# Performance work log

Measured on AMD Instinct MI355X. Metric: run time of the kernel, lower is better.

## Reference

```python
import jax, jax.numpy as jnp
import numpy as np

N_FRAME = 100000
N_TFN = 25000
E = 2000000
NUM_RBF = 16
D_MIN, D_MAX = 0.0, 20.0
EPS = 1e-8


def _rbf(d):
    # GVP-style radial basis: [E] -> [E, NUM_RBF]
    mu = jnp.linspace(D_MIN, D_MAX, NUM_RBF, dtype=d.dtype)
    sigma = (D_MAX - D_MIN) / NUM_RBF
    return jnp.exp(-(((d[..., None] - mu) / sigma) ** 2))


def _sh(vec, dist):
    # component-normalized real spherical harmonics l=0,1,2 on unit vectors
    # (normalize=True, normalization='component': ||Y_l||^2 = 2l+1)
    r = vec / dist[..., None]
    x, y, z = r[..., 0], r[..., 1], r[..., 2]
    s3 = 1.7320508075688772   # sqrt(3)
    s5 = 2.23606797749979     # sqrt(5)
    s15 = 3.872983346207417   # sqrt(15)
    l0 = jnp.ones_like(x)
    sh = jnp.stack([
        l0,
        s3 * x, s3 * y, s3 * z,
        s15 * x * y,
        s15 * y * z,
        0.5 * s5 * (3.0 * z * z - 1.0),
        s15 * x * z,
        0.5 * s15 * (x * x - y * y),
    ], axis=-1)  # [E, 9]
    return sh


def _edge_feats(vec):
    # eps-shifted norm, exactly as torch.linalg.vector_norm(vec + eps)
    d = jnp.linalg.norm(vec + EPS, axis=-1)  # [E]
    return jnp.concatenate([_rbf(d), _sh(vec, d)], axis=-1)  # [E, NUM_RBF+9]


def setup_inputs() -> dict:
    key = jax.random.key(0)
    k1, k2, k3, k4 = jax.random.split(key, 4)
    trans = jax.random.normal(k1, (N_FRAME, 3), dtype=jnp.float32) * 10.0
    f2t = jax.random.randint(k2, (2, E), 0, N_TFN)
    t2t = jax.random.randint(k3, (2, E), 0, N_TFN)
    t2f = jax.random.randint(k4, (2, E), 0, N_TFN)
    return {"trans": trans, "frame2tfn_edge_index": f2t,
            "tfn2tfn_edge_index": t2t, "tfn2frame_edge_index": t2f,
            "n_tfn": N_TFN}


def reference(trans, frame2tfn_edge_index, tfn2tfn_edge_index, tfn2frame_edge_index, n_tfn):
    f_src, t_dst = frame2tfn_edge_index[0], frame2tfn_edge_index[1]
    # scatter-mean of frame translations onto coarse (tfn) nodes
    sums = jax.ops.segment_sum(trans[f_src], t_dst, num_segments=n_tfn)  # [n_tfn, 3]
    cnt = jax.ops.segment_sum(jnp.ones((f_src.shape[0],), trans.dtype), t_dst,
                              num_segments=n_tfn)
    tfn_x = sums / jnp.maximum(cnt, 1.0)[:, None]
    # per-edge-type gather -> distance vecs -> RBF + SH
    f2t_vec = trans[f_src] - tfn_x[t_dst]
    t2t_vec = tfn_x[tfn2tfn_edge_index[0]] - tfn_x[tfn2tfn_edge_index[1]]
    t2f_vec = tfn_x[tfn2frame_edge_index[0]] - trans[tfn2frame_edge_index[1]]
    out = jnp.stack([_edge_feats(f2t_vec), _edge_feats(t2t_vec),
                     _edge_feats(t2f_vec)], axis=0)  # [3, E, NUM_RBF+9]
    return out
```

## Files before the change

### kernel.cpp

```cpp
#include <hip/hip_runtime.h>

constexpr int BLK = 256;
constexpr float D_MIN = 0.0f, D_MAX = 20.0f;
constexpr int NUM_RBF = 16;
constexpr float EPS = 1e-8f;

constexpr double FP_SCALE = 1073741824.0;
constexpr double FP_INV = 1.0 / 1073741824.0;

__global__ __launch_bounds__(BLK) void scatter_kernel(
    const float* __restrict__ trans,
    const int* __restrict__ f2t,
    long long* __restrict__ sums,
    int* __restrict__ cnt,
    int E)
{
    int e = blockIdx.x * BLK + threadIdx.x;
    if (e >= E) return;
    int src = f2t[e];
    int dst = f2t[e + E];
    float x = trans[src * 3 + 0];
    float y = trans[src * 3 + 1];
    float z = trans[src * 3 + 2];
    unsigned long long* s = (unsigned long long*)(sums + (size_t)dst * 3);
    atomicAdd(s + 0, (unsigned long long)llrint((double)x * FP_SCALE));
    atomicAdd(s + 1, (unsigned long long)llrint((double)y * FP_SCALE));
    atomicAdd(s + 2, (unsigned long long)llrint((double)z * FP_SCALE));
    atomicAdd(cnt + dst, 1);
}

__global__ __launch_bounds__(BLK) void finalize_kernel(
    const long long* __restrict__ sums,
    const int* __restrict__ cnt,
    float* __restrict__ tfn_x,
    int n_tfn)
{
    int i = blockIdx.x * BLK + threadIdx.x;
    if (i >= n_tfn) return;
    float c = fmaxf((float)cnt[i], 1.0f);
    #pragma unroll
    for (int k = 0; k < 3; ++k) {
        float s = (float)((double)sums[i * 3 + k] * FP_INV);
        tfn_x[i * 3 + k] = s / c;
    }
}

__global__ __launch_bounds__(BLK) void edge_feats_kernel(
    const float* __restrict__ trans,
    const float* __restrict__ tfn_x,
    const int* __restrict__ f2t,
    const int* __restrict__ t2t,
    const int* __restrict__ t2f,
    float* __restrict__ out,
    int E)
{
    __shared__ float smem[BLK * 25];

    const int typ = blockIdx.y;
    const int e0 = blockIdx.x * BLK;
    const int e = e0 + threadIdx.x;

    if (e < E) {
        float ax, ay, az, bx, by, bz;
        if (typ == 0) {
            int i0 = f2t[e], i1 = f2t[e + E];
            ax = trans[i0 * 3 + 0]; ay = trans[i0 * 3 + 1]; az = trans[i0 * 3 + 2];
            bx = tfn_x[i1 * 3 + 0]; by = tfn_x[i1 * 3 + 1]; bz = tfn_x[i1 * 3 + 2];
        } else if (typ == 1) {
            int i0 = t2t[e], i1 = t2t[e + E];
            ax = tfn_x[i0 * 3 + 0]; ay = tfn_x[i0 * 3 + 1]; az = tfn_x[i0 * 3 + 2];
            bx = tfn_x[i1 * 3 + 0]; by = tfn_x[i1 * 3 + 1]; bz = tfn_x[i1 * 3 + 2];
        } else {
            int i0 = t2f[e], i1 = t2f[e + E];
            ax = tfn_x[i0 * 3 + 0]; ay = tfn_x[i0 * 3 + 1]; az = tfn_x[i0 * 3 + 2];
            bx = trans[i1 * 3 + 0]; by = trans[i1 * 3 + 1]; bz = trans[i1 * 3 + 2];
        }
        float vx = ax - bx, vy = ay - by, vz = az - bz;

        float dx = vx + EPS, dy = vy + EPS, dz = vz + EPS;
        float d = sqrtf(dx * dx + dy * dy + dz * dz);

        float* row = smem + threadIdx.x * 25;

        constexpr float MU_STEP = (D_MAX - D_MIN) / (NUM_RBF - 1);
        #pragma unroll
        for (int i = 0; i < NUM_RBF; ++i) {
            float t = (d - (float)i * MU_STEP) * 0.8f;
            row[i] = expf(-(t * t));
        }

        float rx = vx / d, ry = vy / d, rz = vz / d;
        const float s3 = 1.7320508075688772f;
        const float s5 = 2.23606797749979f;
        const float s15 = 3.872983346207417f;
        row[16] = 1.0f;
        row[17] = s3 * rx;
        row[18] = s3 * ry;
        row[19] = s3 * rz;
        row[20] = s15 * rx * ry;
        row[21] = s15 * ry * rz;
        row[22] = 0.5f * s5 * (3.0f * rz * rz - 1.0f);
        row[23] = s15 * rx * rz;
        row[24] = 0.5f * s15 * (rx * rx - ry * ry);
    }
    __syncthreads();

    const int cnt_e = min(BLK, E - e0);
    const int total = cnt_e * 25;
    const size_t base = ((size_t)typ * E + e0) * 25;
    float4* out4 = (float4*)(out + base);
    const float4* s4 = (const float4*)smem;
    const int total4 = total >> 2;
    for (int i = threadIdx.x; i < total4; i += BLK) out4[i] = s4[i];
    for (int i = (total4 << 2) + threadIdx.x; i < total; i += BLK) out[base + i] = smem[i];
}

extern "C" void kernel_launch(void* const* d_in, const int* in_sizes, int n_in,
                              void* d_out, int out_size, void* d_ws, size_t ws_size,
                              hipStream_t stream) {
    const float* trans = (const float*)d_in[0];
    const int* f2t = (const int*)d_in[1];
    const int* t2t = (const int*)d_in[2];
    const int* t2f = (const int*)d_in[3];
    const int n_tfn = 25000;
    const int E = in_sizes[1] / 2;

    float* out = (float*)d_out;

    long long* sums = (long long*)d_ws;
    int* cnt = (int*)((char*)d_ws + (size_t)n_tfn * 3 * 8);
    float* tfn_x = (float*)((char*)d_ws + (size_t)n_tfn * 3 * 8 + (size_t)n_tfn * 4);

    hipMemsetAsync(d_ws, 0, (size_t)n_tfn * 3 * 8 + (size_t)n_tfn * 4, stream);

    const int nblk_e = (E + BLK - 1) / BLK;
    scatter_kernel<<<nblk_e, BLK, 0, stream>>>(trans, f2t, sums, cnt, E);
    finalize_kernel<<<(n_tfn + BLK - 1) / BLK, BLK, 0, stream>>>(sums, cnt, tfn_x, n_tfn);

    dim3 grid(nblk_e, 3);
    edge_feats_kernel<<<grid, BLK, 0, stream>>>(trans, tfn_x, f2t, t2t, t2f, out, E);
}
```

Baseline: 1.001 ms.

## Replicate scatter accumulators to cut atomic contention; use fast exp and reciprocal

The scatter-mean now writes into 32 replicated copies of the fixed-point sum and count arrays, chosen by block index, and the finalize kernel reduces across the copies. This aims to spread atomics over more addresses and lower contention on hot tfn nodes. In exchange it needs a 32x larger memset, more workspace and a longer reduction. The edge kernel also uses branchless pointer selection, __expf in place of expf, and one reciprocal instead of three divides, which may change precision slightly.

After: 1.002 ms. About the same (+0.1%).

```diff
diff --git a/kernel.cpp b/kernel.cpp
--- a/kernel.cpp
+++ b/kernel.cpp
@@ -4,6 +4,7 @@
 constexpr float D_MIN = 0.0f, D_MAX = 20.0f;
 constexpr int NUM_RBF = 16;
 constexpr float EPS = 1e-8f;
+constexpr int NREP = 32;
 
 constexpr double FP_SCALE = 1073741824.0;
 constexpr double FP_INV = 1.0 / 1073741824.0;
@@ -13,20 +14,22 @@
     const int* __restrict__ f2t,
     long long* __restrict__ sums,
     int* __restrict__ cnt,
-    int E)
+    int E, int n_tfn)
 {
     int e = blockIdx.x * BLK + threadIdx.x;
     if (e >= E) return;
+    int rep = blockIdx.x & (NREP - 1);
     int src = f2t[e];
     int dst = f2t[e + E];
     float x = trans[src * 3 + 0];
     float y = trans[src * 3 + 1];
     float z = trans[src * 3 + 2];
-    unsigned long long* s = (unsigned long long*)(sums + (size_t)dst * 3);
+    unsigned long long* s =
+        (unsigned long long*)(sums + ((size_t)rep * n_tfn + dst) * 3);
     atomicAdd(s + 0, (unsigned long long)llrint((double)x * FP_SCALE));
     atomicAdd(s + 1, (unsigned long long)llrint((double)y * FP_SCALE));
     atomicAdd(s + 2, (unsigned long long)llrint((double)z * FP_SCALE));
-    atomicAdd(cnt + dst, 1);
+    atomicAdd(cnt + rep * n_tfn + dst, 1);
 }
 
 __global__ __launch_bounds__(BLK) void finalize_kernel(
@@ -37,12 +40,18 @@
 {
     int i = blockIdx.x * BLK + threadIdx.x;
     if (i >= n_tfn) return;
-    float c = fmaxf((float)cnt[i], 1.0f);
-    #pragma unroll
-    for (int k = 0; k < 3; ++k) {
-        float s = (float)((double)sums[i * 3 + k] * FP_INV);
-        tfn_x[i * 3 + k] = s / c;
+    long long sx = 0, sy = 0, sz = 0;
+    int c = 0;
+    #pragma unroll 4
+    for (int r = 0; r < NREP; ++r) {
+        const long long* p = sums + ((size_t)r * n_tfn + i) * 3;
+        sx += p[0]; sy += p[1]; sz += p[2];
+        c += cnt[r * n_tfn + i];
     }
+    float fc = fmaxf((float)c, 1.0f);
+    tfn_x[i * 3 + 0] = (float)((double)sx * FP_INV) / fc;
+    tfn_x[i * 3 + 1] = (float)((double)sy * FP_INV) / fc;
+    tfn_x[i * 3 + 2] = (float)((double)sz * FP_INV) / fc;
 }
 
 __global__ __launch_bounds__(BLK) void edge_feats_kernel(
@@ -61,20 +70,13 @@
     const int e = e0 + threadIdx.x;
 
     if (e < E) {
-        float ax, ay, az, bx, by, bz;
-        if (typ == 0) {
-            int i0 = f2t[e], i1 = f2t[e + E];
-            ax = trans[i0 * 3 + 0]; ay = trans[i0 * 3 + 1]; az = trans[i0 * 3 + 2];
-            bx = tfn_x[i1 * 3 + 0]; by = tfn_x[i1 * 3 + 1]; bz = tfn_x[i1 * 3 + 2];
-        } else if (typ == 1) {
-            int i0 = t2t[e], i1 = t2t[e + E];
-            ax = tfn_x[i0 * 3 + 0]; ay = tfn_x[i0 * 3 + 1]; az = tfn_x[i0 * 3 + 2];
-            bx = tfn_x[i1 * 3 + 0]; by = tfn_x[i1 * 3 + 1]; bz = tfn_x[i1 * 3 + 2];
-        } else {
-            int i0 = t2f[e], i1 = t2f[e + E];
-            ax = tfn_x[i0 * 3 + 0]; ay = tfn_x[i0 * 3 + 1]; az = tfn_x[i0 * 3 + 2];
-            bx = trans[i1 * 3 + 0]; by = trans[i1 * 3 + 1]; bz = trans[i1 * 3 + 2];
-        }
+        const int* idx = (typ == 0) ? f2t : (typ == 1) ? t2t : t2f;
+        const float* abase = (typ == 0) ? trans : tfn_x;
+        const float* bbase = (typ == 2) ? trans : tfn_x;
+        int i0 = idx[e], i1 = idx[e + E];
+        float ax = abase[i0 * 3 + 0], ay = abase[i0 * 3 + 1], az = abase[i0 * 3 + 2];
+        float bx = bbase[i1 * 3 + 0], by = bbase[i1 * 3 + 1], bz = bbase[i1 * 3 + 2];
+
         float vx = ax - bx, vy = ay - by, vz = az - bz;
 
         float dx = vx + EPS, dy = vy + EPS, dz = vz + EPS;
@@ -86,10 +88,11 @@
         #pragma unroll
         for (int i = 0; i < NUM_RBF; ++i) {
             float t = (d - (float)i * MU_STEP) * 0.8f;
-            row[i] = expf(-(t * t));
+            row[i] = __expf(-(t * t));
         }
 
-        float rx = vx / d, ry = vy / d, rz = vz / d;
+        float inv_d = 1.0f / d;
+        float rx = vx * inv_d, ry = vy * inv_d, rz = vz * inv_d;
         const float s3 = 1.7320508075688772f;
         const float s5 = 2.23606797749979f;
         const float s15 = 3.872983346207417f;
@@ -127,14 +130,16 @@
 
     float* out = (float*)d_out;
 
+    const size_t sums_bytes = (size_t)NREP * n_tfn * 3 * 8;
+    const size_t cnt_bytes  = (size_t)NREP * n_tfn * 4;
     long long* sums = (long long*)d_ws;
-    int* cnt = (int*)((char*)d_ws + (size_t)n_tfn * 3 * 8);
-    float* tfn_x = (float*)((char*)d_ws + (size_t)n_tfn * 3 * 8 + (size_t)n_tfn * 4);
+    int* cnt = (int*)((char*)d_ws + sums_bytes);
+    float* tfn_x = (float*)((char*)d_ws + sums_bytes + cnt_bytes);
 
-    hipMemsetAsync(d_ws, 0, (size_t)n_tfn * 3 * 8 + (size_t)n_tfn * 4, stream);
+    hipMemsetAsync(d_ws, 0, sums_bytes + cnt_bytes, stream);
 
     const int nblk_e = (E + BLK - 1) / BLK;
-    scatter_kernel<<<nblk_e, BLK, 0, stream>>>(trans, f2t, sums, cnt, E);
+    scatter_kernel<<<nblk_e, BLK, 0, stream>>>(trans, f2t, sums, cnt, E, n_tfn);
     finalize_kernel<<<(n_tfn + BLK - 1) / BLK, BLK, 0, stream>>>(sums, cnt, tfn_x, n_tfn);
 
     dim3 grid(nblk_e, 3);
```
